# Kernel optimization log

Measured on AMD Instinct MI355X. Metric: run time of the kernel, lower is better.

## Reference

```python
import jax, jax.numpy as jnp
import numpy as np

N_SERIES = 32768
N_TIME = 512
SEAS = 24
MAX_NUM_SERIES = 32768
OUTPUT_SIZE = 7


def setup_inputs() -> dict:
    key = jax.random.key(0)
    k1, k2, k3, k4, k5 = jax.random.split(key, 5)
    # y must be strictly positive (divisions and logs of levels)
    y = jax.random.uniform(k1, (N_SERIES, N_TIME), jnp.float32) + 0.5
    idxs = jax.random.randint(k2, (N_SERIES,), 0, MAX_NUM_SERIES)
    lev_sms = jax.random.normal(k3, (MAX_NUM_SERIES, 1), jnp.float32) * 0.5
    seas_sms = jax.random.normal(k4, (MAX_NUM_SERIES, 1), jnp.float32) * 0.5
    init_seas = jax.random.normal(k5, (MAX_NUM_SERIES, SEAS), jnp.float32) * 0.1
    return {
        "y": y,
        "idxs": idxs,
        "lev_sms": lev_sms,
        "seas_sms": seas_sms,
        "init_seas": init_seas,
        "seasonality": SEAS,
        "output_size": OUTPUT_SIZE,
    }


def _es_forward(y, idxs, lev_sms_p, seas_sms_p, init_seas_p, seasonality, output_size):
    n_series, n_time = y.shape
    lev_sms = jax.nn.sigmoid(lev_sms_p[idxs, 0])          # (n,)
    # NOTE: faithful to original code, which (buggy or not) derives seas_sms
    # from self.lev_sms as well; seas_sms_p is an unused parameter.
    seas_sms = jax.nn.sigmoid(lev_sms_p[idxs, 0])         # (n,)
    init_seas = jnp.exp(init_seas_p[idxs, :])             # (n, seasonality)

    lev0 = y[:, 0] / init_seas[:, 0]                      # levels[:,0]

    # Ring-buffer formulation of the lag-`seasonality` recurrence:
    # original reads seasonalities[:, t] and writes seasonalities[:, t+seasonality];
    # both map to slot t % seasonality (read-before-write). Initial buffer slots
    # equal init_seas columns (slot 0 = init_seas[:,0], which also covers the
    # duplicated entry seasonalities[:, seasonality]).
    positions = jnp.arange(1, n_time) % seasonality       # (n_time-1,)
    y_steps = y[:, 1:].T                                  # (n_time-1, n)

    def step(carry, xs):
        lev_prev, buf = carry                             # (n,), (n, seasonality)
        y_t, pos = xs
        seas_t = buf[:, pos]
        newlev = lev_sms * (y_t / seas_t) + (1.0 - lev_sms) * lev_prev
        newseason = seas_sms * (y_t / newlev) + (1.0 - seas_sms) * seas_t
        log_diff = jnp.log(newlev) - jnp.log(lev_prev)
        buf = buf.at[:, pos].set(newseason)
        return (newlev, buf), (newlev, newseason, log_diff)

    _, (levs, seasons, logd) = jax.lax.scan(step, (lev0, init_seas), (y_steps, positions))

    levels = jnp.concatenate([lev0[:, None], levs.T], axis=1)              # (n, n_time)
    seasonalities = jnp.concatenate(
        [init_seas, init_seas[:, :1], seasons.T], axis=1                   # (n, seasonality+n_time)
    )
    log_diff_of_levels = logd.T                                            # (n, n_time-1)

    if output_size > seasonality:
        # faithful to original (which uses len(seasonalities) == n_series)
        start = seasonalities.shape[0] - seasonality
        end = start + output_size - seasonality
        seasonalities = jnp.concatenate([seasonalities, seasonalities[:, start:end]], axis=1)

    return levels, seasonalities, log_diff_of_levels


def reference(y, idxs, lev_sms, seas_sms, init_seas, seasonality, output_size):
    return _es_forward(y, idxs, lev_sms, seas_sms, init_seas, seasonality, output_size)
```

## Files before the change

kernel.cpp:

```cpp
#include <hip/hip_runtime.h>

#define NT 512
#define SEASN 24
#define TT 48

constexpr int SEA_STRIDE = NT + SEASN;
constexpr int LOG_STRIDE = NT - 1;
constexpr float LN2 = 0.6931471805599453f;

__device__ __forceinline__ float frcp(float x)  { return __builtin_amdgcn_rcpf(x); }
__device__ __forceinline__ float flog2(float x) { return __builtin_amdgcn_logf(x); }

__device__ __forceinline__ void gl_lds4(const float* g, float* lds) {
    __builtin_amdgcn_global_load_lds(
        (const __attribute__((address_space(1))) void*)g,
        (__attribute__((address_space(3))) void*)lds, 4, 0, 0);
}

struct State { float lev, l2prev; };

template<int T, bool FIRST>
__device__ __forceinline__ void compute_tile(const float* __restrict__ ybuf,
                                             float2* __restrict__ c2,
                                             float* __restrict__ dtile,
                                             int lane, float lsm,
                                             float (&buf)[SEASN], State& st)
{
    #pragma unroll
    for (int k = 0; k < T; ++k) {
        const int pos = k % SEASN;
        const float yt = ybuf[lane * 49 + k];
        if (FIRST && k == 0) {
            st.lev = yt * frcp(buf[0]);
            st.l2prev = flog2(st.lev);
            c2[lane] = make_float2(st.lev, buf[0]);
        } else {
            const float sv = buf[pos];
            const float nl = st.lev + lsm * (yt * frcp(sv) - st.lev);
            const float ns = sv + lsm * (yt * frcp(nl) - sv);
            const float l2 = flog2(nl);
            c2[k * 65 + lane] = make_float2(nl, ns);
            dtile[k * 65 + lane] = (l2 - st.l2prev) * LN2;
            st.l2prev = l2; st.lev = nl; buf[pos] = ns;
        }
    }
}

__device__ __forceinline__ void flush_tile(const float2* __restrict__ c2,
                                           const float* __restrict__ dtile,
                                           int lane, int sbase, int tbase, int T,
                                           float* __restrict__ levels,
                                           float* __restrict__ seasv,
                                           float* __restrict__ logd)
{
    if (lane < T) {
        #pragma unroll 16
        for (int r = 0; r < 64; ++r) {
            const size_t srow = (size_t)(sbase + r);
            const float2 ls = c2[lane * 65 + r];
            const float dv = dtile[lane * 65 + r];
            levels[srow * NT + tbase + lane] = ls.x;
            seasv[srow * SEA_STRIDE + SEASN + tbase + lane] = ls.y;
            if (tbase + lane > 0)
                logd[srow * LOG_STRIDE + tbase + lane - 1] = dv;
        }
    }
}

__global__ __launch_bounds__(64)
void es_fwd(const float* __restrict__ y, const int* __restrict__ idxs,
            const float* __restrict__ lev_sms_p, const float* __restrict__ init_seas_p,
            float* __restrict__ levels, float* __restrict__ seasv,
            float* __restrict__ logd)
{
    __shared__ float ybuf[64 * 49];
    __shared__ __align__(16) float2 c2[TT * 65];
    __shared__ float dtile[TT * 65];

    const int lane = threadIdx.x;
    const int sbase = blockIdx.x * 64;
    const int s = sbase + lane;
    const int idx = idxs[s];
    const float lsm = frcp(1.0f + __expf(-lev_sms_p[idx]));

    float buf[SEASN];
    {
        float* searow = seasv + (size_t)s * SEA_STRIDE;
        const float4* is4 = (const float4*)(init_seas_p + (size_t)idx * SEASN);
        #pragma unroll
        for (int g = 0; g < 6; ++g) {
            float4 v = is4[g];
            float a = __expf(v.x), b = __expf(v.y), c = __expf(v.z), d = __expf(v.w);
            buf[4*g]=a; buf[4*g+1]=b; buf[4*g+2]=c; buf[4*g+3]=d;
            float4 o; o.x=a; o.y=b; o.z=c; o.w=d;
            ((float4*)searow)[g] = o;
        }
    }

    const float* ysrc = y + (size_t)sbase * NT + lane;
    auto stage = [&](int tbase, int cols) {
        if (lane < cols) {
            const float* g = ysrc + tbase;
            #pragma unroll
            for (int r = 0; r < 64; ++r)
                gl_lds4(g + (size_t)r * NT, &ybuf[r * 49]);
        }
    };

    State st;

    stage(0, TT);
    __builtin_amdgcn_s_waitcnt(0);
    compute_tile<TT, true>(ybuf, c2, dtile, lane, lsm, buf, st);

    stage(TT, TT);
    flush_tile(c2, dtile, lane, sbase, 0, TT, levels, seasv, logd);
    __builtin_amdgcn_s_waitcnt(0);

    for (int m = 1; m <= 9; ++m) {
        compute_tile<TT, false>(ybuf, c2, dtile, lane, lsm, buf, st);
        if (m < 9) stage((m + 1) * TT, TT);
        else       stage(480, 32);
        flush_tile(c2, dtile, lane, sbase, m * TT, TT, levels, seasv, logd);
        __builtin_amdgcn_s_waitcnt(0);
    }

    compute_tile<32, false>(ybuf, c2, dtile, lane, lsm, buf, st);
    flush_tile(c2, dtile, lane, sbase, 480, 32, levels, seasv, logd);
}

extern "C" void kernel_launch(void* const* d_in, const int* in_sizes, int n_in,
                              void* d_out, int out_size, void* d_ws, size_t ws_size,
                              hipStream_t stream)
{
    const float* y         = (const float*)d_in[0];
    const int*   idxs      = (const int*)d_in[1];
    const float* lev_sms   = (const float*)d_in[2];
    const float* init_seas = (const float*)d_in[4];
    const int n_series = in_sizes[1];

    float* levels = (float*)d_out;
    float* seasv  = levels + (size_t)n_series * NT;
    float* logdv  = seasv  + (size_t)n_series * SEA_STRIDE;

    es_fwd<<<n_series / 64, 64, 0, stream>>>(y, idxs, lev_sms, init_seas,
                                             levels, seasv, logdv);
}
```

Before: 346.8 us.

## Use 64-step tiles with float4 row-major writeback and separate LDS tiles

Raises the time tile from 48 to 64 steps, so the 512-step series splits into 8 equal tiles. The seasonal ring position is handled with a compile-time phase per tile. Results now go into per-series row-major LDS tiles (stride 65). They are flushed with 16-lane x 4-row float4 global stores instead of scalar column-at-a-time stores, and the init-season row is also written vectorised through LDS. The goal is wider, more coalesced global writes and fewer store instructions. In exchange it uses more LDS per block, which may lower occupancy, and it uses unaligned scalar stores for the log-diff output.

```diff
diff --git a/kernel.cpp b/kernel.cpp
--- a/kernel.cpp
+++ b/kernel.cpp
@@ -2,7 +2,8 @@
 
 #define NT 512
 #define SEASN 24
-#define TT 48
+#define TT 64
+#define YS 65
 
 constexpr int SEA_STRIDE = NT + SEASN;
 constexpr int LOG_STRIDE = NT - 1;
@@ -17,52 +18,57 @@
         (__attribute__((address_space(3))) void*)lds, 4, 0, 0);
 }
 
-struct State { float lev, l2prev; };
-
-template<int T, bool FIRST>
-__device__ __forceinline__ void compute_tile(const float* __restrict__ ybuf,
-                                             float2* __restrict__ c2,
-                                             float* __restrict__ dtile,
-                                             int lane, float lsm,
-                                             float (&buf)[SEASN], State& st)
+template<int PHASE, bool FIRST>
+__device__ __forceinline__ void compute_tile(const float* __restrict__ yb,
+                                             float* __restrict__ lt,
+                                             float* __restrict__ st,
+                                             float* __restrict__ dt,
+                                             float lsm, float (&buf)[SEASN],
+                                             float& lev, float& l2p)
 {
     #pragma unroll
-    for (int k = 0; k < T; ++k) {
-        const int pos = k % SEASN;
-        const float yt = ybuf[lane * 49 + k];
+    for (int k = 0; k < TT; ++k) {
+        const int pos = (PHASE + k) % SEASN;
+        const float yt = yb[k];
         if (FIRST && k == 0) {
-            st.lev = yt * frcp(buf[0]);
-            st.l2prev = flog2(st.lev);
-            c2[lane] = make_float2(st.lev, buf[0]);
+            lev = yt * frcp(buf[0]);
+            l2p = flog2(lev);
+            lt[0] = lev;
+            st[0] = buf[0];
         } else {
             const float sv = buf[pos];
-            const float nl = st.lev + lsm * (yt * frcp(sv) - st.lev);
+            const float nl = lev + lsm * (yt * frcp(sv) - lev);
             const float ns = sv + lsm * (yt * frcp(nl) - sv);
             const float l2 = flog2(nl);
-            c2[k * 65 + lane] = make_float2(nl, ns);
-            dtile[k * 65 + lane] = (l2 - st.l2prev) * LN2;
-            st.l2prev = l2; st.lev = nl; buf[pos] = ns;
+            lt[k] = nl; st[k] = ns; dt[k] = (l2 - l2p) * LN2;
+            l2p = l2; lev = nl; buf[pos] = ns;
         }
     }
 }
 
-__device__ __forceinline__ void flush_tile(const float2* __restrict__ c2,
-                                           const float* __restrict__ dtile,
-                                           int lane, int sbase, int tbase, int T,
+template<bool FIRSTTILE>
+__device__ __forceinline__ void flush_tile(const float* __restrict__ lt,
+                                           const float* __restrict__ st,
+                                           const float* __restrict__ dt,
+                                           int q, int rr, int sbase, int tbase,
                                            float* __restrict__ levels,
                                            float* __restrict__ seasv,
                                            float* __restrict__ logd)
 {
-    if (lane < T) {
-        #pragma unroll 16
-        for (int r = 0; r < 64; ++r) {
-            const size_t srow = (size_t)(sbase + r);
-            const float2 ls = c2[lane * 65 + r];
-            const float dv = dtile[lane * 65 + r];
-            levels[srow * NT + tbase + lane] = ls.x;
-            seasv[srow * SEA_STRIDE + SEASN + tbase + lane] = ls.y;
-            if (tbase + lane > 0)
-                logd[srow * LOG_STRIDE + tbase + lane - 1] = dv;
+    #pragma unroll
+    for (int i = 0; i < 16; ++i) {
+        const int r = 4 * i + rr;
+        const size_t srow = (size_t)(sbase + r);
+        const int off = r * YS + 4 * q;
+        float4 lv = make_float4(lt[off], lt[off+1], lt[off+2], lt[off+3]);
+        float4 sv = make_float4(st[off], st[off+1], st[off+2], st[off+3]);
+        *(float4*)(levels + srow * NT + tbase + 4 * q) = lv;
+        *(float4*)(seasv + srow * SEA_STRIDE + SEASN + tbase + 4 * q) = sv;
+        float* dp = logd + srow * LOG_STRIDE + tbase + 4 * q - 1;
+        if (FIRSTTILE && q == 0) {
+            dp[1] = dt[off+1]; dp[2] = dt[off+2]; dp[3] = dt[off+3];
+        } else {
+            dp[0] = dt[off]; dp[1] = dt[off+1]; dp[2] = dt[off+2]; dp[3] = dt[off+3];
         }
     }
 }
@@ -73,60 +79,79 @@
             float* __restrict__ levels, float* __restrict__ seasv,
             float* __restrict__ logd)
 {
-    __shared__ float ybuf[64 * 49];
-    __shared__ __align__(16) float2 c2[TT * 65];
-    __shared__ float dtile[TT * 65];
+    __shared__ float ybuf [64 * YS];
+    __shared__ float ltile[64 * YS];
+    __shared__ float stile[64 * YS];
+    __shared__ float dtile[64 * YS];
 
-    const int lane = threadIdx.x;
+    const int lane  = threadIdx.x;
     const int sbase = blockIdx.x * 64;
-    const int s = sbase + lane;
-    const int idx = idxs[s];
+    const int q  = lane & 15;
+    const int rr = lane >> 4;
+
+    auto stage = [&](int m) {
+        const float* g = y + (size_t)sbase * NT + m * TT + lane;
+        #pragma unroll
+        for (int r = 0; r < 64; ++r)
+            gl_lds4(g + (size_t)r * NT, &ybuf[r * YS]);
+    };
+
+    stage(0);
+
+    const int idx = idxs[sbase + lane];
     const float lsm = frcp(1.0f + __expf(-lev_sms_p[idx]));
 
     float buf[SEASN];
     {
-        float* searow = seasv + (size_t)s * SEA_STRIDE;
         const float4* is4 = (const float4*)(init_seas_p + (size_t)idx * SEASN);
         #pragma unroll
         for (int g = 0; g < 6; ++g) {
             float4 v = is4[g];
-            float a = __expf(v.x), b = __expf(v.y), c = __expf(v.z), d = __expf(v.w);
-            buf[4*g]=a; buf[4*g+1]=b; buf[4*g+2]=c; buf[4*g+3]=d;
-            float4 o; o.x=a; o.y=b; o.z=c; o.w=d;
-            ((float4*)searow)[g] = o;
+            buf[4*g+0] = __expf(v.x); buf[4*g+1] = __expf(v.y);
+            buf[4*g+2] = __expf(v.z); buf[4*g+3] = __expf(v.w);
+            #pragma unroll
+            for (int j = 0; j < 4; ++j)
+                ltile[lane * YS + 4*g + j] = buf[4*g+j];
         }
     }
 
-    const float* ysrc = y + (size_t)sbase * NT + lane;
-    auto stage = [&](int tbase, int cols) {
-        if (lane < cols) {
-            const float* g = ysrc + tbase;
-            #pragma unroll
-            for (int r = 0; r < 64; ++r)
-                gl_lds4(g + (size_t)r * NT, &ybuf[r * 49]);
+    if (q < 6) {
+        #pragma unroll
+        for (int i = 0; i < 16; ++i) {
+            const int r = 4 * i + rr;
+            const size_t srow = (size_t)(sbase + r);
+            const int off = r * YS + 4 * q;
+            float4 v = make_float4(ltile[off], ltile[off+1], ltile[off+2], ltile[off+3]);
+            *(float4*)(seasv + srow * SEA_STRIDE + 4 * q) = v;
         }
-    };
+    }
 
-    State st;
+    float lev, l2p;
+    const float* yb = &ybuf[lane * YS];
+    float* lt = &ltile[lane * YS];
+    float* st = &stile[lane * YS];
+    float* dt = &dtile[lane * YS];
 
-    stage(0, TT);
     __builtin_amdgcn_s_waitcnt(0);
-    compute_tile<TT, true>(ybuf, c2, dtile, lane, lsm, buf, st);
-
-    stage(TT, TT);
-    flush_tile(c2, dtile, lane, sbase, 0, TT, levels, seasv, logd);
+    compute_tile<0, true >(yb, lt, st, dt, lsm, buf, lev, l2p);
+    stage(1);
+    flush_tile<true >(ltile, stile, dtile, q, rr, sbase, 0 * TT, levels, seasv, logd);
     __builtin_amdgcn_s_waitcnt(0);
 
-    for (int m = 1; m <= 9; ++m) {
-        compute_tile<TT, false>(ybuf, c2, dtile, lane, lsm, buf, st);
-        if (m < 9) stage((m + 1) * TT, TT);
-        else       stage(480, 32);
-        flush_tile(c2, dtile, lane, sbase, m * TT, TT, levels, seasv, logd);
-        __builtin_amdgcn_s_waitcnt(0);
-    }
+#define TILE(M, PHASE, LAST) \
+    compute_tile<PHASE, false>(yb, lt, st, dt, lsm, buf, lev, l2p); \
+    if (!(LAST)) stage((M) + 1); \
+    flush_tile<false>(ltile, stile, dtile, q, rr, sbase, (M) * TT, levels, seasv, logd); \
+    if (!(LAST)) __builtin_amdgcn_s_waitcnt(0);
 
-    compute_tile<32, false>(ybuf, c2, dtile, lane, lsm, buf, st);
-    flush_tile(c2, dtile, lane, sbase, 480, 32, levels, seasv, logd);
+    TILE(1, 16, false)
+    TILE(2,  8, false)
+    TILE(3,  0, false)
+    TILE(4, 16, false)
+    TILE(5,  8, false)
+    TILE(6,  0, false)
+    TILE(7, 16, true)
+#undef TILE
 }
 
 extern "C" void kernel_launch(void* const* d_in, const int* in_sizes, int n_in,
```

New measurement: 329.5 us. -5.0%, faster.
